# Kernel optimization log

Measured on AMD Instinct MI355X. Metric: run time of the kernel, lower is better.

## Reference

```python
import jax, jax.numpy as jnp
import numpy as np

BATCH = 4096
IN_DIM = 2048      # pooled CNN feature dim
OUT_DIM = 14951    # landmark classes
EPS = 1e-12        # tf.nn.l2_normalize epsilon


def _hadamard_slice(rows, cols):
    # Sylvester Hadamard entry: H[i, j] = (-1)^popcount(i & j).
    # Builds only the [rows, cols] slice of the 16384x16384 matrix.
    i = jnp.arange(rows, dtype=jnp.uint32)[:, None]
    j = jnp.arange(cols, dtype=jnp.uint32)[None, :]
    par = jax.lax.population_count(i & j) & 1
    return 1.0 - 2.0 * par.astype(jnp.float32)


def setup_inputs() -> dict:
    key = jax.random.key(0)
    k1, k2 = jax.random.split(key)
    x = jax.random.normal(k1, (BATCH, IN_DIM), dtype=jnp.float32)
    init_scale = 1.0 / np.sqrt(OUT_DIM)
    scale = jnp.full((1,), init_scale, dtype=jnp.float32)
    bias = jax.random.uniform(k2, (OUT_DIM,), dtype=jnp.float32,
                              minval=-init_scale, maxval=init_scale)
    return {"x": x, "scale": scale, "bias": bias}


def reference(x, scale, bias):
    H = _hadamard_slice(x.shape[1], bias.shape[0])  # [IN_DIM, OUT_DIM], +-1
    # L2-normalize along last axis (matches K.l2_normalize / tf.nn.l2_normalize)
    xn = x * jax.lax.rsqrt(jnp.maximum(jnp.sum(x * x, axis=-1, keepdims=True), EPS))
    out = -scale * jnp.matmul(xn, H) + bias  # activation=None
    return out
```

## Files before the change

kernel.cpp:

```cpp
#include <hip/hip_runtime.h>

#define BATCH   4096
#define IN_DIM  2048
#define OUT_DIM 14951
#define ROWS    4
#define NT      512
#define STRIDE  2052
#define EPS     1e-12f

typedef float nfloat4 __attribute__((ext_vector_type(4)));

__global__ __launch_bounds__(NT, 8) void HadamardClassifier_44487271252814_kernel(
    const float* __restrict__ x,
    const float* __restrict__ scale,
    const float* __restrict__ bias,
    float* __restrict__ out)
{
    __shared__ float y[ROWS * STRIDE];
    __shared__ float rss[ROWS * 2];
    __shared__ float srow[ROWS];

    const int tid = threadIdx.x;
    const int r   = tid >> 7;
    const int t   = tid & 127;
    const int b0  = blockIdx.x * ROWS;

    const float4* xv = reinterpret_cast<const float4*>(x + (size_t)(b0 + r) * IN_DIM) + 4 * t;
    float4 v0 = xv[0], v1 = xv[1], v2 = xv[2], v3 = xv[3];
    float a[16] = { v0.x, v0.y, v0.z, v0.w, v1.x, v1.y, v1.z, v1.w,
                    v2.x, v2.y, v2.z, v2.w, v3.x, v3.y, v3.z, v3.w };

    float ss = 0.f;
    #pragma unroll
    for (int k = 0; k < 16; ++k) ss += a[k] * a[k];
    #pragma unroll
    for (int off = 32; off > 0; off >>= 1) ss += __shfl_down(ss, off, 64);
    if ((tid & 63) == 0) rss[tid >> 6] = ss;

    #pragma unroll
    for (int h = 1; h < 16; h <<= 1) {
        #pragma unroll
        for (int g = 0; g < 16; g += 2 * h) {
            #pragma unroll
            for (int k = 0; k < h; ++k) {
                float u = a[g + k], w = a[g + k + h];
                a[g + k]     = u + w;
                a[g + k + h] = u - w;
            }
        }
    }

    #pragma unroll
    for (int s = 0; s < 6; ++s) {
        const float sgn = (t & (1 << s)) ? -1.0f : 1.0f;
        #pragma unroll
        for (int k = 0; k < 16; ++k) {
            float recv = __shfl_xor(a[k], 1 << s, 64);
            a[k] = fmaf(sgn, a[k], recv);
        }
    }

    float* yr = y + r * STRIDE;
    #pragma unroll
    for (int k = 0; k < 4; ++k)
        *reinterpret_cast<float4*>(&yr[16 * t + 4 * k]) =
            make_float4(a[4 * k], a[4 * k + 1], a[4 * k + 2], a[4 * k + 3]);
    __syncthreads();

    if (tid < ROWS)
        srow[tid] = -scale[0] * rsqrtf(fmaxf(rss[2 * tid] + rss[2 * tid + 1], EPS));

    const int tp = t ^ 64;
    float p[16];
    #pragma unroll
    for (int k = 0; k < 4; ++k) {
        float4 w = *reinterpret_cast<const float4*>(&yr[16 * tp + 4 * k]);
        p[4 * k] = w.x; p[4 * k + 1] = w.y; p[4 * k + 2] = w.z; p[4 * k + 3] = w.w;
    }
    __syncthreads();

    const float sg = (t < 64) ? 1.0f : -1.0f;
    #pragma unroll
    for (int k = 0; k < 16; ++k) a[k] = fmaf(sg, a[k], p[k]);

    #pragma unroll
    for (int k = 0; k < 4; ++k)
        *reinterpret_cast<float4*>(&yr[16 * t + 4 * k]) =
            make_float4(a[4 * k], a[4 * k + 1], a[4 * k + 2], a[4 * k + 3]);
    if (t == 0)
        *reinterpret_cast<float4*>(&yr[2048]) = make_float4(a[0], a[1], a[2], a[3]);
    __syncthreads();

    const float sv0 = srow[0], sv1 = srow[1], sv2 = srow[2], sv3 = srow[3];
    const float* y0p = y;
    const float* y1p = y + STRIDE;
    const float* y2p = y + 2 * STRIDE;
    const float* y3p = y + 3 * STRIDE;

    for (int k = tid; k < (OUT_DIM >> 2) - 1; k += NT) {
        const int e  = 4 * k;
        const int m4 = e & (IN_DIM - 1);
        const float4 blo = *reinterpret_cast<const float4*>(&bias[e]);
        const float4 bhi = *reinterpret_cast<const float4*>(&bias[e + 4]);
        const size_t ob = (size_t)b0 * OUT_DIM + e;

        {
            const float4 w0 = *reinterpret_cast<const float4*>(&y0p[m4]);
            nfloat4 o;
            o.x = fmaf(sv0, w0.x, blo.x);
            o.y = fmaf(sv0, w0.y, blo.y);
            o.z = fmaf(sv0, w0.z, blo.z);
            o.w = fmaf(sv0, w0.w, blo.w);
            __builtin_nontemporal_store(o, reinterpret_cast<nfloat4*>(&out[ob]));
        }
        {
            const float4 w0 = *reinterpret_cast<const float4*>(&y1p[m4]);
            const float4 w1 = *reinterpret_cast<const float4*>(&y1p[m4 + 4]);
            nfloat4 o;
            o.x = fmaf(sv1, w0.y, blo.y);
            o.y = fmaf(sv1, w0.z, blo.z);
            o.z = fmaf(sv1, w0.w, blo.w);
            o.w = fmaf(sv1, w1.x, bhi.x);
            __builtin_nontemporal_store(o, reinterpret_cast<nfloat4*>(&out[ob + OUT_DIM + 1]));
        }
        {
            const float4 w0 = *reinterpret_cast<const float4*>(&y2p[m4]);
            const float4 w1 = *reinterpret_cast<const float4*>(&y2p[m4 + 4]);
            nfloat4 o;
            o.x = fmaf(sv2, w0.z, blo.z);
            o.y = fmaf(sv2, w0.w, blo.w);
            o.z = fmaf(sv2, w1.x, bhi.x);
            o.w = fmaf(sv2, w1.y, bhi.y);
            __builtin_nontemporal_store(o, reinterpret_cast<nfloat4*>(&out[ob + 2 * OUT_DIM + 2]));
        }
        {
            const float4 w0 = *reinterpret_cast<const float4*>(&y3p[m4]);
            const float4 w1 = *reinterpret_cast<const float4*>(&y3p[m4 + 4]);
            nfloat4 o;
            o.x = fmaf(sv3, w0.w, blo.w);
            o.y = fmaf(sv3, w1.x, bhi.x);
            o.z = fmaf(sv3, w1.y, bhi.y);
            o.w = fmaf(sv3, w1.z, bhi.z);
            __builtin_nontemporal_store(o, reinterpret_cast<nfloat4*>(&out[ob + 3 * OUT_DIM + 3]));
        }
    }

    if (tid < 28) {
        const int rr  = tid / 7;
        const int idx = tid - rr * 7;
        const int j   = (idx < rr) ? idx : (14944 + idx);
        out[(size_t)(b0 + rr) * OUT_DIM + j] =
            fmaf(srow[rr], y[rr * STRIDE + (j & (IN_DIM - 1))], bias[j]);
    }
}

extern "C" void kernel_launch(void* const* d_in, const int* in_sizes, int n_in,
                              void* d_out, int out_size, void* d_ws, size_t ws_size,
                              hipStream_t stream) {
    const float* x     = (const float*)d_in[0];
    const float* scale = (const float*)d_in[1];
    const float* bias  = (const float*)d_in[2];
    float* out = (float*)d_out;

    hipLaunchKernelGGL(HadamardClassifier_44487271252814_kernel,
                       dim3(BATCH / ROWS), dim3(NT), 0, stream,
                       x, scale, bias, out);
}
```

Baseline: 289.8 us.

## Split into FWHT kernel writing workspace and per-row output-expansion kernel

The fused kernel is split into two launches when workspace is available. The first kernel computes the Hadamard transform and per-row scale and writes them to global workspace. The second kernel runs one block per batch row to expand the output, which gives far more blocks and a simpler store pattern. This adds a 32MB workspace write and read plus an extra launch in exchange for better parallelism in the store-bound phase.

Result: slower. 298.9 us (+3.1%).

```diff
diff --git a/kernel.cpp b/kernel.cpp
--- a/kernel.cpp
+++ b/kernel.cpp
@@ -4,21 +4,21 @@
 #define IN_DIM  2048
 #define OUT_DIM 14951
 #define ROWS    4
-#define NT      512
+#define NT1     512
+#define NT2     256
 #define STRIDE  2052
 #define EPS     1e-12f
 
 typedef float nfloat4 __attribute__((ext_vector_type(4)));
 
-__global__ __launch_bounds__(NT, 8) void HadamardClassifier_44487271252814_kernel(
+__global__ __launch_bounds__(NT1, 4) void HC_fwht_kernel(
     const float* __restrict__ x,
     const float* __restrict__ scale,
-    const float* __restrict__ bias,
-    float* __restrict__ out)
+    float* __restrict__ wy,
+    float* __restrict__ wscale)
 {
-    __shared__ float y[ROWS * STRIDE];
+    __shared__ float y[ROWS * IN_DIM];
     __shared__ float rss[ROWS * 2];
-    __shared__ float srow[ROWS];
 
     const int tid = threadIdx.x;
     const int r   = tid >> 7;
@@ -60,6 +60,136 @@
         }
     }
 
+    float* yr = y + r * IN_DIM;
+    #pragma unroll
+    for (int k = 0; k < 4; ++k)
+        *reinterpret_cast<float4*>(&yr[16 * t + 4 * k]) =
+            make_float4(a[4 * k], a[4 * k + 1], a[4 * k + 2], a[4 * k + 3]);
+    __syncthreads();
+
+    if (tid < ROWS)
+        wscale[b0 + tid] = -scale[0] * rsqrtf(fmaxf(rss[2 * tid] + rss[2 * tid + 1], EPS));
+
+    const int   tp = t ^ 64;
+    const float sg = (t < 64) ? 1.0f : -1.0f;
+    float4* wrow = reinterpret_cast<float4*>(wy + (size_t)(b0 + r) * IN_DIM);
+    #pragma unroll
+    for (int k = 0; k < 4; ++k) {
+        float4 w = *reinterpret_cast<const float4*>(&yr[16 * tp + 4 * k]);
+        float4 o;
+        o.x = fmaf(sg, a[4 * k],     w.x);
+        o.y = fmaf(sg, a[4 * k + 1], w.y);
+        o.z = fmaf(sg, a[4 * k + 2], w.z);
+        o.w = fmaf(sg, a[4 * k + 3], w.w);
+        wrow[4 * t + k] = o;
+    }
+}
+
+template<int C>
+__device__ __forceinline__ void hc_out_body(const float* __restrict__ yl,
+                                            const float* __restrict__ bias,
+                                            float* __restrict__ orow, float sv)
+{
+    for (int k = threadIdx.x; k < 3736; k += NT2) {
+        const int m4 = (4 * k) & (IN_DIM - 1);
+        const float4 w0  = *reinterpret_cast<const float4*>(&yl[m4]);
+        const float4 w1  = *reinterpret_cast<const float4*>(&yl[m4 + 4]);
+        const float4 blo = *reinterpret_cast<const float4*>(&bias[4 * k]);
+        const float4 bhi = *reinterpret_cast<const float4*>(&bias[4 * k + 4]);
+        const float wv[8] = { w0.x, w0.y, w0.z, w0.w, w1.x, w1.y, w1.z, w1.w };
+        const float bv[8] = { blo.x, blo.y, blo.z, blo.w, bhi.x, bhi.y, bhi.z, bhi.w };
+        nfloat4 o;
+        o.x = fmaf(sv, wv[C + 0], bv[C + 0]);
+        o.y = fmaf(sv, wv[C + 1], bv[C + 1]);
+        o.z = fmaf(sv, wv[C + 2], bv[C + 2]);
+        o.w = fmaf(sv, wv[C + 3], bv[C + 3]);
+        __builtin_nontemporal_store(o, reinterpret_cast<nfloat4*>(&orow[C + 4 * k]));
+    }
+}
+
+__global__ __launch_bounds__(NT2, 8) void HC_out_kernel(
+    const float* __restrict__ wy,
+    const float* __restrict__ wscale,
+    const float* __restrict__ bias,
+    float* __restrict__ out)
+{
+    __shared__ float yl[IN_DIM + 8];
+    const int b   = blockIdx.x;
+    const int tid = threadIdx.x;
+
+    const float4* src  = reinterpret_cast<const float4*>(wy + (size_t)b * IN_DIM);
+    float4*       dst4 = reinterpret_cast<float4*>(yl);
+    float4 t0 = src[tid], t1 = src[tid + NT2];
+    dst4[tid] = t0;
+    dst4[tid + NT2] = t1;
+    if (tid == 0) dst4[512] = t0;
+    const float sv = wscale[b];
+    __syncthreads();
+
+    float* orow = out + (size_t)b * OUT_DIM;
+    switch (b & 3) {
+        case 0: hc_out_body<0>(yl, bias, orow, sv); break;
+        case 1: hc_out_body<1>(yl, bias, orow, sv); break;
+        case 2: hc_out_body<2>(yl, bias, orow, sv); break;
+        default: hc_out_body<3>(yl, bias, orow, sv); break;
+    }
+
+    const int C = b & 3;
+    if (tid < 7) {
+        const int j = (tid < C) ? tid : (C + 14944 + (tid - C));
+        orow[j] = fmaf(sv, yl[j & (IN_DIM - 1)], bias[j]);
+    }
+}
+
+__global__ __launch_bounds__(NT1, 8) void HadamardClassifier_44487271252814_kernel(
+    const float* __restrict__ x,
+    const float* __restrict__ scale,
+    const float* __restrict__ bias,
+    float* __restrict__ out)
+{
+    __shared__ float y[ROWS * STRIDE];
+    __shared__ float rss[ROWS * 2];
+    __shared__ float srow[ROWS];
+
+    const int tid = threadIdx.x;
+    const int r   = tid >> 7;
+    const int t   = tid & 127;
+    const int b0  = blockIdx.x * ROWS;
+
+    const float4* xv = reinterpret_cast<const float4*>(x + (size_t)(b0 + r) * IN_DIM) + 4 * t;
+    float4 v0 = xv[0], v1 = xv[1], v2 = xv[2], v3 = xv[3];
+    float a[16] = { v0.x, v0.y, v0.z, v0.w, v1.x, v1.y, v1.z, v1.w,
+                    v2.x, v2.y, v2.z, v2.w, v3.x, v3.y, v3.z, v3.w };
+
+    float ss = 0.f;
+    #pragma unroll
+    for (int k = 0; k < 16; ++k) ss += a[k] * a[k];
+    #pragma unroll
+    for (int off = 32; off > 0; off >>= 1) ss += __shfl_down(ss, off, 64);
+    if ((tid & 63) == 0) rss[tid >> 6] = ss;
+
+    #pragma unroll
+    for (int h = 1; h < 16; h <<= 1) {
+        #pragma unroll
+        for (int g = 0; g < 16; g += 2 * h) {
+            #pragma unroll
+            for (int k = 0; k < h; ++k) {
+                float u = a[g + k], w = a[g + k + h];
+                a[g + k]     = u + w;
+                a[g + k + h] = u - w;
+            }
+        }
+    }
+    #pragma unroll
+    for (int s = 0; s < 6; ++s) {
+        const float sgn = (t & (1 << s)) ? -1.0f : 1.0f;
+        #pragma unroll
+        for (int k = 0; k < 16; ++k) {
+            float recv = __shfl_xor(a[k], 1 << s, 64);
+            a[k] = fmaf(sgn, a[k], recv);
+        }
+    }
+
     float* yr = y + r * STRIDE;
     #pragma unroll
     for (int k = 0; k < 4; ++k)
@@ -97,13 +227,12 @@
     const float* y2p = y + 2 * STRIDE;
     const float* y3p = y + 3 * STRIDE;
 
-    for (int k = tid; k < (OUT_DIM >> 2) - 1; k += NT) {
+    for (int k = tid; k < (OUT_DIM >> 2) - 1; k += NT1) {
         const int e  = 4 * k;
         const int m4 = e & (IN_DIM - 1);
         const float4 blo = *reinterpret_cast<const float4*>(&bias[e]);
         const float4 bhi = *reinterpret_cast<const float4*>(&bias[e + 4]);
         const size_t ob = (size_t)b0 * OUT_DIM + e;
-
         {
             const float4 w0 = *reinterpret_cast<const float4*>(&y0p[m4]);
             nfloat4 o;
@@ -162,7 +291,17 @@
     const float* bias  = (const float*)d_in[2];
     float* out = (float*)d_out;
 
-    hipLaunchKernelGGL(HadamardClassifier_44487271252814_kernel,
-                       dim3(BATCH / ROWS), dim3(NT), 0, stream,
-                       x, scale, bias, out);
-}
+    const size_t ws_needed = (size_t)BATCH * IN_DIM * sizeof(float) + BATCH * sizeof(float);
+    if (d_ws && ws_size >= ws_needed) {
+        float* wy     = (float*)d_ws;
+        float* wscale = (float*)d_ws + (size_t)BATCH * IN_DIM;
+        hipLaunchKernelGGL(HC_fwht_kernel, dim3(BATCH / ROWS), dim3(NT1), 0, stream,
+                           x, scale, wy, wscale);
+        hipLaunchKernelGGL(HC_out_kernel, dim3(BATCH), dim3(NT2), 0, stream,
+                           wy, wscale, bias, out);
+    } else {
+        hipLaunchKernelGGL(HadamardClassifier_44487271252814_kernel,
+                           dim3(BATCH / ROWS), dim3(NT1), 0, stream,
+                           x, scale, bias, out);
+    }
+}
```
